# Kernel optimization log

Hardware: AMD Instinct MI355X
Metric: run time of the kernel (lower is better)

Reference implementation:

```python
import jax, jax.numpy as jnp
import numpy as np

N, F_NODE, DIM, H, K, OUT, L = 200000, 16, 3, 128, 20, 4, 4


def setup_inputs() -> dict:
    key = jax.random.key(0)
    ks = jax.random.split(key, 10)
    x = jax.random.normal(ks[0], (N, F_NODE), jnp.float32)
    pos = jax.random.normal(ks[1], (N, DIM), jnp.float32)
    y = jax.random.normal(ks[2], (DIM,), jnp.float32)
    # eigenvector-like basis, roughly orthonormal columns scale
    phi = jax.random.normal(ks[3], (N, K), jnp.float32) / np.sqrt(N).astype(np.float32)
    # torch Linear convention: W is [out, in], y = x @ W.T + b
    lift_w = jax.random.normal(ks[4], (H, F_NODE + 2 * DIM), jnp.float32) * 0.05
    lift_b = jnp.zeros((H,), jnp.float32)
    lin_w = jax.random.normal(ks[5], (L, H, H), jnp.float32) * 0.05  # per-layer, bias=False
    kernel = jax.random.normal(ks[6], (L, K, H, H), jnp.float32) * 0.05
    lower_w = jax.random.normal(ks[7], (OUT, H), jnp.float32) * 0.05
    lower_b = jnp.zeros((OUT,), jnp.float32)
    return dict(x=x, pos=pos, y=y, phi=phi, lift_w=lift_w, lift_b=lift_b,
                lin_w=lin_w, kernel=kernel, lower_w=lower_w, lower_b=lower_b)


def reference(x, pos, y, phi, lift_w, lift_b, lin_w, kernel, lower_w, lower_b):
    # lift: concat node feats, positions, broadcast global y -> [N, F_NODE+2*DIM]
    h = jnp.concatenate([x, pos, y * jnp.ones_like(pos)], axis=1) @ lift_w.T + lift_b
    # pinv(phi) is identical every layer in the original; compute once. [K, N]
    phi_pinv = jnp.linalg.pinv(phi)
    for l in range(L):
        v = phi_pinv @ h                              # [K, H] spectral coefficients
        rv = jnp.einsum('kij,kj->ki', kernel[l], v)   # batched mode matvec (= nested vmap)
        h = jax.nn.elu(h @ lin_w[l].T + phi @ rv)     # [N, H]
    return h @ lower_w.T + lower_b                    # [N, OUT]
```

## Files before the change

kernel.cpp:

```cpp
#include <hip/hip_runtime.h>
#include <math.h>

#define Nn 200000
#define NT 3125

typedef __attribute__((ext_vector_type(8))) short short8;
typedef __attribute__((ext_vector_type(16))) float floatx16;

#define SWZ4(row, g) (((g) ^ ((row) & 7)) << 2)

__device__ __forceinline__ unsigned rnbf(float x) {
    unsigned u = __builtin_bit_cast(unsigned, x);
    return (u + 0x7fffu + ((u >> 16) & 1u)) >> 16;
}
__device__ __forceinline__ float asf(unsigned u) { return __builtin_bit_cast(float, u); }
__device__ __forceinline__ unsigned packf(float x) {
    unsigned hb = rnbf(x);
    float fh = asf(hb << 16);
    unsigned lb = rnbf(x - fh);
    return hb | (lb << 16);
}
__device__ __forceinline__ float unpackf(unsigned p) {
    return asf(p << 16) + asf(p & 0xffff0000u);
}
__device__ __forceinline__ void permsplit(const unsigned* e, short8& hi, short8& lo) {
    uint4 h, l;
    h.x = __builtin_amdgcn_perm(e[1], e[0], 0x05040100u);
    h.y = __builtin_amdgcn_perm(e[3], e[2], 0x05040100u);
    h.z = __builtin_amdgcn_perm(e[5], e[4], 0x05040100u);
    h.w = __builtin_amdgcn_perm(e[7], e[6], 0x05040100u);
    l.x = __builtin_amdgcn_perm(e[1], e[0], 0x07060302u);
    l.y = __builtin_amdgcn_perm(e[3], e[2], 0x07060302u);
    l.z = __builtin_amdgcn_perm(e[5], e[4], 0x07060302u);
    l.w = __builtin_amdgcn_perm(e[7], e[6], 0x07060302u);
    hi = __builtin_bit_cast(short8, h);
    lo = __builtin_bit_cast(short8, l);
}
__device__ __forceinline__ void permsplit2(uint4 q0, uint4 q1, short8& hi, short8& lo) {
    unsigned e[8] = { q0.x, q0.y, q0.z, q0.w, q1.x, q1.y, q1.z, q1.w };
    permsplit(e, hi, lo);
}

__device__ __forceinline__ void pt_accum(const unsigned* As, const unsigned* Ph,
                                         float* __restrict__ PTc_blk, int t) {
    int lane = t & 63, w = t >> 6;
    int ln = lane & 31, hw = lane >> 5;
    int j0 = w * 32;
    floatx16 ap;
#pragma unroll
    for (int i = 0; i < 16; i++) ap[i] = 0.f;
#pragma unroll
    for (int ks = 0; ks < 4; ks++) {
        unsigned pa[8], e[8];
#pragma unroll
        for (int j = 0; j < 8; j++) {
            int node = ks * 16 + 8 * hw + j;
            pa[j] = Ph[node * 32 + SWZ4(node, ln >> 2) + (ln & 3)];
            int col = j0 + ln;
            e[j] = As[node * 128 + SWZ4(node, col >> 2) + (col & 3)];
        }
        short8 a_hi, a_lo, b_hi, b_lo;
        permsplit(pa, a_hi, a_lo);
        permsplit(e, b_hi, b_lo);
        ap = __builtin_amdgcn_mfma_f32_32x32x16_bf16(a_hi, b_hi, ap, 0, 0, 0);
        ap = __builtin_amdgcn_mfma_f32_32x32x16_bf16(a_lo, b_hi, ap, 0, 0, 0);
        ap = __builtin_amdgcn_mfma_f32_32x32x16_bf16(a_hi, b_lo, ap, 0, 0, 0);
    }
#pragma unroll
    for (int r = 0; r < 16; r++) {
        int mode = (r & 3) + 8 * (r >> 2) + 4 * hw;
        if (mode < 20) unsafeAtomicAdd(&PTc_blk[mode * 128 + j0 + ln], ap[r]);
    }
}

__global__ void ptreduce_k(const float* __restrict__ PTc, float* __restrict__ PT) {
    int j = blockIdx.x * 128 + threadIdx.x;
    float s0 = 0.f, s1 = 0.f, s2 = 0.f, s3 = 0.f;
#pragma unroll
    for (int c = 0; c < 64; c += 4) {
        s0 += PTc[(size_t)c * 2560 + j];
        s1 += PTc[(size_t)(c + 1) * 2560 + j];
        s2 += PTc[(size_t)(c + 2) * 2560 + j];
        s3 += PTc[(size_t)(c + 3) * 2560 + j];
    }
    PT[j] = (s0 + s1) + (s2 + s3);
}

__global__ void bias_fold_k(const float* __restrict__ y, const float* __restrict__ lw,
                            const float* __restrict__ lb, float* __restrict__ b2) {
    int j = threadIdx.x;
    float s = lb[j];
#pragma unroll
    for (int d = 0; d < 3; d++) s += y[d] * lw[j * 22 + 19 + d];
    b2[j] = s;
}

__global__ void wsplit_k(const float* __restrict__ lw, const float* __restrict__ low_w,
                         unsigned short* __restrict__ Wh, unsigned short* __restrict__ Wl,
                         unsigned short* __restrict__ LWh, unsigned short* __restrict__ LWl) {
    int i = blockIdx.x * 256 + threadIdx.x;
    float w;
    unsigned short *ph, *pl;
    int idx;
    if (i < 65536) { w = lw[i]; ph = Wh; pl = Wl; idx = i; }
    else           { w = low_w[i - 65536]; ph = LWh; pl = LWl; idx = i - 65536; }
    unsigned hb = rnbf(w);
    float fh = asf(hb << 16);
    unsigned lb = rnbf(w - fh);
    ph[idx] = (unsigned short)hb;
    pl[idx] = (unsigned short)lb;
}

__global__ __launch_bounds__(256) void lift_k(const float* __restrict__ x,
                                              const float* __restrict__ pos,
                                              const float* __restrict__ phi,
                                              const float* __restrict__ lw,
                                              const float* __restrict__ b2,
                                              unsigned* __restrict__ hpk,
                                              float* __restrict__ PTc) {
    __shared__ union {
        struct { float xs[64][21]; float Wc[20][132]; } a;
        unsigned As[64 * 128];
    } sm;
    __shared__ unsigned Ph[64 * 32];
    int t = threadIdx.x;
    int n0 = blockIdx.x * 64;
    {
        int n = t >> 2, f4 = (t & 3) * 4;
        float4 xv = *(const float4*)(x + (size_t)(n0 + n) * 16 + f4);
        sm.a.xs[n][f4 + 0] = xv.x; sm.a.xs[n][f4 + 1] = xv.y;
        sm.a.xs[n][f4 + 2] = xv.z; sm.a.xs[n][f4 + 3] = xv.w;
    }
    if (t < 192) { int n = t / 3, d = t % 3; sm.a.xs[n][16 + d] = pos[(size_t)(n0 + n) * 3 + d]; }
    if (t < 64) sm.a.xs[t][19] = 1.f;
    for (int idx = t; idx < 2560; idx += 256) {
        int k = idx >> 7, j = idx & 127;
        sm.a.Wc[k][j] = (k < 19) ? lw[j * 22 + k] : b2[j];
    }
    for (int idx = t; idx < 2048; idx += 256) {
        int row = idx >> 5, kk = idx & 31;
        float pv = (kk < 20) ? phi[(size_t)(n0 + row) * 20 + kk] : 0.f;
        Ph[row * 32 + SWZ4(row, kk >> 2) + (kk & 3)] = packf(pv);
    }
    __syncthreads();
    int tx = t & 31, ty = t >> 5, i0 = tx * 4;
    float acc[8][4];
#pragma unroll
    for (int m = 0; m < 8; m++)
#pragma unroll
        for (int c = 0; c < 4; c++) acc[m][c] = 0.f;
#pragma unroll 4
    for (int k = 0; k < 20; k++) {
        float4 w = *(const float4*)&sm.a.Wc[k][i0];
#pragma unroll
        for (int m = 0; m < 8; m++) {
            float a = sm.a.xs[ty + 8 * m][k];
            acc[m][0] += a * w.x; acc[m][1] += a * w.y;
            acc[m][2] += a * w.z; acc[m][3] += a * w.w;
        }
    }
    __syncthreads();
#pragma unroll
    for (int m = 0; m < 8; m++) {
        uint4 o;
        o.x = packf(acc[m][0]); o.y = packf(acc[m][1]);
        o.z = packf(acc[m][2]); o.w = packf(acc[m][3]);
        int row = ty + 8 * m;
        *(uint4*)&hpk[(size_t)(n0 + row) * 128 + i0] = o;
        *(uint4*)&sm.As[row * 128 + SWZ4(row, tx)] = o;
    }
    __syncthreads();
    pt_accum(sm.As, Ph, PTc + (size_t)(blockIdx.x & 63) * 2560, t);
}

__global__ void gram_k(const float* __restrict__ phi, float* __restrict__ G) {
    __shared__ float ph[64 * 20];
    int t = threadIdx.x;
    int i0 = t / 20, j0 = t % 20;
    int p1 = t + 256;
    int i1 = p1 / 20, j1 = p1 % 20;
    float a0 = 0.f, a1 = 0.f;
    for (int tile = blockIdx.x; tile < NT; tile += gridDim.x) {
        const float* src = phi + tile * 1280;
        for (int idx = t; idx < 1280; idx += 256) ph[idx] = src[idx];
        __syncthreads();
        for (int n = 0; n < 64; n++) {
            const float* r = ph + n * 20;
            a0 += r[i0] * r[j0];
            if (p1 < 400) a1 += r[i1] * r[j1];
        }
        __syncthreads();
    }
    unsafeAtomicAdd(&G[t], a0);
    if (p1 < 400) unsafeAtomicAdd(&G[p1], a1);
}

__global__ void ginv_k(const float* __restrict__ G, float* __restrict__ Gi) {
    __shared__ float A[20][40];
    __shared__ float colp[20];
    __shared__ float piv;
    int t = threadIdx.x;
    for (int idx = t; idx < 400; idx += 64) {
        int r = idx / 20, c = idx % 20;
        A[r][c] = G[idx];
        A[r][c + 20] = (r == c) ? 1.f : 0.f;
    }
    __syncthreads();
    for (int p = 0; p < 20; p++) {
        if (t == 0) piv = 1.f / A[p][p];
        __syncthreads();
        for (int c = t; c < 40; c += 64) A[p][c] *= piv;
        __syncthreads();
        if (t < 20) colp[t] = A[t][p];
        __syncthreads();
        for (int e = t; e < 800; e += 64) {
            int r = e / 40, c = e % 40;
            if (r != p) A[r][c] -= colp[r] * A[p][c];
        }
        __syncthreads();
    }
    for (int idx = t; idx < 400; idx += 64) {
        int r = idx / 20, c = idx % 20;
        Gi[idx] = A[r][c + 20];
    }
}

__global__ void rv_k(const float* __restrict__ Gi, const float* __restrict__ PT,
                     const float* __restrict__ kern_l,
                     unsigned short* __restrict__ RVh, unsigned short* __restrict__ RVl) {
    __shared__ __align__(16) float v[128];
    __shared__ float part[128];
    int k = blockIdx.x;
    int t = threadIdx.x;
    if (t < 128) {
        const float* gr = Gi + k * 20;
        float s = 0.f;
#pragma unroll
        for (int m = 0; m < 20; m++) s += gr[m] * PT[m * 128 + t];
        v[t] = s;
    }
    __syncthreads();
    int i = t & 127, half = t >> 7;
    const float* kr = kern_l + (size_t)(k * 128 + i) * 128 + half * 64;
    const float* vk = v + half * 64;
    float acc = 0.f;
#pragma unroll 4
    for (int jj = 0; jj < 64; jj += 4) {
        float4 kv = *(const float4*)(kr + jj);
        float4 vv = *(const float4*)(vk + jj);
        acc += kv.x * vv.x + kv.y * vv.y + kv.z * vv.z + kv.w * vv.w;
    }
    if (half) part[i] = acc;
    __syncthreads();
    if (!half) {
        float rv = acc + part[i];
        unsigned hb = rnbf(rv);
        float fh = asf(hb << 16);
        unsigned lb = rnbf(rv - fh);
        RVh[i * 32 + k] = (unsigned short)hb;
        RVl[i * 32 + k] = (unsigned short)lb;
    }
}

__global__ __launch_bounds__(256, 4) void update_k(unsigned* __restrict__ hpk,
                                                   const float* __restrict__ phi,
                                                   const unsigned short* __restrict__ Wh,
                                                   const unsigned short* __restrict__ Wl,
                                                   const unsigned short* __restrict__ RVh,
                                                   const unsigned short* __restrict__ RVl,
                                                   float* __restrict__ ptn,
                                                   const unsigned short* __restrict__ LWh,
                                                   const unsigned short* __restrict__ LWl,
                                                   const float* __restrict__ low_b,
                                                   float* __restrict__ outp) {
    __shared__ __align__(16) unsigned As[64 * 128];
    __shared__ __align__(16) unsigned Ph[64 * 32];
    int t = threadIdx.x;
    int n0 = blockIdx.x * 64;
    for (int idx = t; idx < 2048; idx += 256) {
        int row = idx >> 5, g = idx & 31;
        uint4 v = *(const uint4*)(hpk + (size_t)(n0 + row) * 128 + g * 4);
        *(uint4*)&As[row * 128 + SWZ4(row, g)] = v;
    }
    for (int idx = t; idx < 2048; idx += 256) {
        int row = idx >> 5, kk = idx & 31;
        float pv = (kk < 20) ? phi[(size_t)(n0 + row) * 20 + kk] : 0.f;
        Ph[row * 32 + SWZ4(row, kk >> 2) + (kk & 3)] = packf(pv);
    }
    __syncthreads();

    int lane = t & 63, w = t >> 6;
    int ln = lane & 31, hw = lane >> 5;
    int r0 = (w >> 1) * 32, ct0 = (w & 1) * 64;
    int arow = r0 + ln;

    floatx16 acc0, acc1;
#pragma unroll
    for (int i = 0; i < 16; i++) { acc0[i] = 0.f; acc1[i] = 0.f; }

    const unsigned short* whp0 = Wh + (size_t)(ct0 + ln) * 128 + 8 * hw;
    const unsigned short* wlp0 = Wl + (size_t)(ct0 + ln) * 128 + 8 * hw;
    const unsigned short* whp1 = whp0 + 32 * 128;
    const unsigned short* wlp1 = wlp0 + 32 * 128;
    const unsigned* abase = As + arow * 128;

    uint4 wh0c = *(const uint4*)(whp0), wl0c = *(const uint4*)(wlp0);
    uint4 wh1c = *(const uint4*)(whp1), wl1c = *(const uint4*)(wlp1);
    uint4 aq0c = *(const uint4*)(abase + SWZ4(arow, 2 * hw));
    uint4 aq1c = *(const uint4*)(abase + SWZ4(arow, 2 * hw + 1));
#pragma unroll
    for (int ks = 0; ks < 8; ks++) {
        uint4 wh0n, wl0n, wh1n, wl1n, aq0n, aq1n;
        if (ks < 7) {
            int k1 = (ks + 1) * 16;
            int ga = 4 * (ks + 1) + 2 * hw;
            wh0n = *(const uint4*)(whp0 + k1); wl0n = *(const uint4*)(wlp0 + k1);
            wh1n = *(const uint4*)(whp1 + k1); wl1n = *(const uint4*)(wlp1 + k1);
            aq0n = *(const uint4*)(abase + SWZ4(arow, ga));
            aq1n = *(const uint4*)(abase + SWZ4(arow, ga + 1));
        }
        short8 a_hi, a_lo;
        permsplit2(aq0c, aq1c, a_hi, a_lo);
        short8 b0h = __builtin_bit_cast(short8, wh0c);
        short8 b0l = __builtin_bit_cast(short8, wl0c);
        short8 b1h = __builtin_bit_cast(short8, wh1c);
        short8 b1l = __builtin_bit_cast(short8, wl1c);
        acc0 = __builtin_amdgcn_mfma_f32_32x32x16_bf16(a_hi, b0h, acc0, 0, 0, 0);
        acc0 = __builtin_amdgcn_mfma_f32_32x32x16_bf16(a_lo, b0h, acc0, 0, 0, 0);
        acc0 = __builtin_amdgcn_mfma_f32_32x32x16_bf16(a_hi, b0l, acc0, 0, 0, 0);
        acc1 = __builtin_amdgcn_mfma_f32_32x32x16_bf16(a_hi, b1h, acc1, 0, 0, 0);
        acc1 = __builtin_amdgcn_mfma_f32_32x32x16_bf16(a_lo, b1h, acc1, 0, 0, 0);
        acc1 = __builtin_amdgcn_mfma_f32_32x32x16_bf16(a_hi, b1l, acc1, 0, 0, 0);
        if (ks < 7) {
            wh0c = wh0n; wl0c = wl0n; wh1c = wh1n; wl1c = wl1n;
            aq0c = aq0n; aq1c = aq1n;
        }
    }

    const unsigned* pbase = Ph + arow * 32;
#pragma unroll
    for (int ks = 0; ks < 2; ks++) {
        int k0 = ks * 16;
        int gr = 4 * ks + 2 * hw;
        uint4 q0 = *(const uint4*)(pbase + SWZ4(arow, gr));
        uint4 q1 = *(const uint4*)(pbase + SWZ4(arow, gr + 1));
        short8 a_hi, a_lo;
        permsplit2(q0, q1, a_hi, a_lo);
        short8 b0h = __builtin_bit_cast(short8, *(const uint4*)(RVh + (size_t)(ct0 + ln) * 32 + k0 + 8 * hw));
        short8 b0l = __builtin_bit_cast(short8, *(const uint4*)(RVl + (size_t)(ct0 + ln) * 32 + k0 + 8 * hw));
        short8 b1h = __builtin_bit_cast(short8, *(const uint4*)(RVh + (size_t)(ct0 + 32 + ln) * 32 + k0 + 8 * hw));
        short8 b1l = __builtin_bit_cast(short8, *(const uint4*)(RVl + (size_t)(ct0 + 32 + ln) * 32 + k0 + 8 * hw));
        acc0 = __builtin_amdgcn_mfma_f32_32x32x16_bf16(a_hi, b0h, acc0, 0, 0, 0);
        acc0 = __builtin_amdgcn_mfma_f32_32x32x16_bf16(a_lo, b0h, acc0, 0, 0, 0);
        acc0 = __builtin_amdgcn_mfma_f32_32x32x16_bf16(a_hi, b0l, acc0, 0, 0, 0);
        acc1 = __builtin_amdgcn_mfma_f32_32x32x16_bf16(a_hi, b1h, acc1, 0, 0, 0);
        acc1 = __builtin_amdgcn_mfma_f32_32x32x16_bf16(a_lo, b1h, acc1, 0, 0, 0);
        acc1 = __builtin_amdgcn_mfma_f32_32x32x16_bf16(a_hi, b1l, acc1, 0, 0, 0);
    }

    unsigned p0[16], p1[16];
#pragma unroll
    for (int r = 0; r < 16; r++) {
        float v0 = acc0[r];
        v0 = v0 > 0.f ? v0 : __expf(v0) - 1.f;
        p0[r] = packf(v0);
        float v1 = acc1[r];
        v1 = v1 > 0.f ? v1 : __expf(v1) - 1.f;
        p1[r] = packf(v1);
    }
    if (!outp) {
#pragma unroll
        for (int r = 0; r < 16; r++) {
            int row = (r & 3) + 8 * (r >> 2) + 4 * hw;
            size_t base = (size_t)(n0 + r0 + row) * 128;
            hpk[base + ct0 + ln] = p0[r];
            hpk[base + ct0 + 32 + ln] = p1[r];
        }
    }
    if (ptn || outp) {
        __syncthreads();
#pragma unroll
        for (int r = 0; r < 16; r++) {
            int row = r0 + (r & 3) + 8 * (r >> 2) + 4 * hw;
            int c0 = ct0 + ln, c1 = ct0 + 32 + ln;
            As[row * 128 + SWZ4(row, c0 >> 2) + (c0 & 3)] = p0[r];
            As[row * 128 + SWZ4(row, c1 >> 2) + (c1 & 3)] = p1[r];
        }
        __syncthreads();
        if (outp) {
            float* scr = (float*)Ph;
            int kh = w & 1;
            floatx16 ap;
#pragma unroll
            for (int i = 0; i < 16; i++) ap[i] = 0.f;
#pragma unroll
            for (int kk = 0; kk < 4; kk++) {
                int ks = kh * 4 + kk;
                int ga = 4 * ks + 2 * hw;
                uint4 q0 = *(const uint4*)(abase + SWZ4(arow, ga));
                uint4 q1 = *(const uint4*)(abase + SWZ4(arow, ga + 1));
                short8 a_hi, a_lo;
                permsplit2(q0, q1, a_hi, a_lo);
                short8 bh = { 0, 0, 0, 0, 0, 0, 0, 0 };
                short8 bl = { 0, 0, 0, 0, 0, 0, 0, 0 };
                if (ln < 4) {
                    bh = __builtin_bit_cast(short8, *(const uint4*)(LWh + ln * 128 + ks * 16 + 8 * hw));
                    bl = __builtin_bit_cast(short8, *(const uint4*)(LWl + ln * 128 + ks * 16 + 8 * hw));
                }
                ap = __builtin_amdgcn_mfma_f32_32x32x16_bf16(a_hi, bh, ap, 0, 0, 0);
                ap = __builtin_amdgcn_mfma_f32_32x32x16_bf16(a_lo, bh, ap, 0, 0, 0);
                ap = __builtin_amdgcn_mfma_f32_32x32x16_bf16(a_hi, bl, ap, 0, 0, 0);
            }
            if (kh == 1 && ln < 4) {
#pragma unroll
                for (int r = 0; r < 16; r++) {
                    int row = (r & 3) + 8 * (r >> 2) + 4 * hw;
                    scr[(w >> 1) * 128 + row * 4 + ln] = ap[r];
                }
            }
            __syncthreads();
            if (kh == 0 && ln < 4) {
                float b = low_b[ln];
#pragma unroll
                for (int r = 0; r < 16; r++) {
                    int row = (r & 3) + 8 * (r >> 2) + 4 * hw;
                    float s = ap[r] + scr[(w >> 1) * 128 + row * 4 + ln] + b;
                    outp[(size_t)(n0 + r0 + row) * 4 + ln] = s;
                }
            }
        } else {
            pt_accum(As, Ph, ptn + (size_t)(blockIdx.x & 63) * 2560, t);
        }
    }
}

extern "C" void kernel_launch(void* const* d_in, const int* in_sizes, int n_in,
                              void* d_out, int out_size, void* d_ws, size_t ws_size,
                              hipStream_t stream) {
    (void)in_sizes; (void)n_in; (void)out_size; (void)ws_size;
    const float* x       = (const float*)d_in[0];
    const float* pos     = (const float*)d_in[1];
    const float* y       = (const float*)d_in[2];
    const float* phi     = (const float*)d_in[3];
    const float* lift_w  = (const float*)d_in[4];
    const float* lift_b  = (const float*)d_in[5];
    const float* lin_w   = (const float*)d_in[6];
    const float* kern    = (const float*)d_in[7];
    const float* lower_w = (const float*)d_in[8];
    const float* lower_b = (const float*)d_in[9];
    float* out = (float*)d_out;

    char* ws = (char*)d_ws;
    unsigned* hpk = (unsigned*)ws;
    size_t off = (size_t)Nn * 128 * 4;
    float* b2  = (float*)(ws + off);       off += 512;
    float* G   = (float*)(ws + off);       off += 1600;
    float* Gi  = (float*)(ws + off);       off += 1600;
    off = (off + 15) & ~(size_t)15;
    float* PT  = (float*)(ws + off);       off += 10240;
    float* PTc = (float*)(ws + off);       off += 64 * 2560 * 4;
    unsigned short* W_hi = (unsigned short*)(ws + off);  off += 131072;
    unsigned short* W_lo = (unsigned short*)(ws + off);  off += 131072;
    unsigned short* RVh  = (unsigned short*)(ws + off);  off += 8192;
    unsigned short* RVl  = (unsigned short*)(ws + off);  off += 8192;
    unsigned short* LWh  = (unsigned short*)(ws + off);  off += 1024;
    unsigned short* LWl  = (unsigned short*)(ws + off);  off += 1024;

    hipMemsetAsync(G, 0, 1600, stream);
    hipMemsetAsync(PTc, 0, 64 * 2560 * 4, stream);
    hipMemsetAsync(RVh, 0, 8192, stream);
    hipMemsetAsync(RVl, 0, 8192, stream);
    bias_fold_k<<<1, 128, 0, stream>>>(y, lift_w, lift_b, b2);
    wsplit_k<<<258, 256, 0, stream>>>(lin_w, lower_w, W_hi, W_lo, LWh, LWl);
    lift_k<<<NT, 256, 0, stream>>>(x, pos, phi, lift_w, b2, hpk, PTc);
    gram_k<<<256, 256, 0, stream>>>(phi, G);
    ginv_k<<<1, 64, 0, stream>>>(G, Gi);
    ptreduce_k<<<20, 128, 0, stream>>>(PTc, PT);

    for (int l = 0; l < 4; l++) {
        rv_k<<<20, 256, 0, stream>>>(Gi, PT, kern + (size_t)l * 20 * 128 * 128, RVh, RVl);
        float* ptc = (l < 3) ? PTc : (float*)nullptr;
        if (ptc) hipMemsetAsync(ptc, 0, 64 * 2560 * 4, stream);
        update_k<<<NT, 256, 0, stream>>>(hpk, phi, W_hi + (size_t)l * 16384,
                                         W_lo + (size_t)l * 16384, RVh, RVl, ptc,
                                         LWh, LWl, lower_b,
                                         (l == 3) ? out : (float*)nullptr);
        if (ptc) ptreduce_k<<<20, 128, 0, stream>>>(PTc, PT);
    }
}
```

Before: 619.7 us.

## Use 512-thread blocks in update kernel with one 32x32 tile per wave

The update kernel now runs 8 waves per 64-node block instead of 4. Each wave computes a single 32x32 output tile, so it needs one accumulator instead of two and drops the explicit register double-buffering of the weight and activation loads. The spectral projection accumulation is split across all 8 waves by node halves, and the final lowering step is restricted to the first 4 waves. This aims to raise parallelism and lower register pressure per wave, at the cost of more atomics in the projection and losing software prefetch of the operand loads.

```diff
diff --git a/kernel.cpp b/kernel.cpp
--- a/kernel.cpp
+++ b/kernel.cpp
@@ -51,6 +51,40 @@
     for (int i = 0; i < 16; i++) ap[i] = 0.f;
 #pragma unroll
     for (int ks = 0; ks < 4; ks++) {
+        unsigned pa[8], e[8];
+#pragma unroll
+        for (int j = 0; j < 8; j++) {
+            int node = ks * 16 + 8 * hw + j;
+            pa[j] = Ph[node * 32 + SWZ4(node, ln >> 2) + (ln & 3)];
+            int col = j0 + ln;
+            e[j] = As[node * 128 + SWZ4(node, col >> 2) + (col & 3)];
+        }
+        short8 a_hi, a_lo, b_hi, b_lo;
+        permsplit(pa, a_hi, a_lo);
+        permsplit(e, b_hi, b_lo);
+        ap = __builtin_amdgcn_mfma_f32_32x32x16_bf16(a_hi, b_hi, ap, 0, 0, 0);
+        ap = __builtin_amdgcn_mfma_f32_32x32x16_bf16(a_lo, b_hi, ap, 0, 0, 0);
+        ap = __builtin_amdgcn_mfma_f32_32x32x16_bf16(a_hi, b_lo, ap, 0, 0, 0);
+    }
+#pragma unroll
+    for (int r = 0; r < 16; r++) {
+        int mode = (r & 3) + 8 * (r >> 2) + 4 * hw;
+        if (mode < 20) unsafeAtomicAdd(&PTc_blk[mode * 128 + j0 + ln], ap[r]);
+    }
+}
+
+__device__ __forceinline__ void pt_accum8(const unsigned* As, const unsigned* Ph,
+                                          float* __restrict__ PTc_blk, int t) {
+    int lane = t & 63, w = t >> 6;
+    int ln = lane & 31, hw = lane >> 5;
+    int j0 = (w & 3) * 32;
+    int nh = w >> 2;
+    floatx16 ap;
+#pragma unroll
+    for (int i = 0; i < 16; i++) ap[i] = 0.f;
+#pragma unroll
+    for (int ks2 = 0; ks2 < 2; ks2++) {
+        int ks = nh * 2 + ks2;
         unsigned pa[8], e[8];
 #pragma unroll
         for (int j = 0; j < 8; j++) {
@@ -262,7 +296,7 @@
     }
 }
 
-__global__ __launch_bounds__(256, 4) void update_k(unsigned* __restrict__ hpk,
+__global__ __launch_bounds__(512, 8) void update_k(unsigned* __restrict__ hpk,
                                                    const float* __restrict__ phi,
                                                    const unsigned short* __restrict__ Wh,
                                                    const unsigned short* __restrict__ Wl,
@@ -277,12 +311,12 @@
     __shared__ __align__(16) unsigned Ph[64 * 32];
     int t = threadIdx.x;
     int n0 = blockIdx.x * 64;
-    for (int idx = t; idx < 2048; idx += 256) {
+    for (int idx = t; idx < 2048; idx += 512) {
         int row = idx >> 5, g = idx & 31;
         uint4 v = *(const uint4*)(hpk + (size_t)(n0 + row) * 128 + g * 4);
         *(uint4*)&As[row * 128 + SWZ4(row, g)] = v;
     }
-    for (int idx = t; idx < 2048; idx += 256) {
+    for (int idx = t; idx < 2048; idx += 512) {
         int row = idx >> 5, kk = idx & 31;
         float pv = (kk < 20) ? phi[(size_t)(n0 + row) * 20 + kk] : 0.f;
         Ph[row * 32 + SWZ4(row, kk >> 2) + (kk & 3)] = packf(pv);
@@ -291,50 +325,32 @@
 
     int lane = t & 63, w = t >> 6;
     int ln = lane & 31, hw = lane >> 5;
-    int r0 = (w >> 1) * 32, ct0 = (w & 1) * 64;
+    int r0 = (w >> 2) * 32, ct0 = (w & 3) * 32;
     int arow = r0 + ln;
 
-    floatx16 acc0, acc1;
-#pragma unroll
-    for (int i = 0; i < 16; i++) { acc0[i] = 0.f; acc1[i] = 0.f; }
-
-    const unsigned short* whp0 = Wh + (size_t)(ct0 + ln) * 128 + 8 * hw;
-    const unsigned short* wlp0 = Wl + (size_t)(ct0 + ln) * 128 + 8 * hw;
-    const unsigned short* whp1 = whp0 + 32 * 128;
-    const unsigned short* wlp1 = wlp0 + 32 * 128;
+    floatx16 acc;
+#pragma unroll
+    for (int i = 0; i < 16; i++) acc[i] = 0.f;
+
+    const unsigned short* whp = Wh + (size_t)(ct0 + ln) * 128 + 8 * hw;
+    const unsigned short* wlp = Wl + (size_t)(ct0 + ln) * 128 + 8 * hw;
     const unsigned* abase = As + arow * 128;
 
-    uint4 wh0c = *(const uint4*)(whp0), wl0c = *(const uint4*)(wlp0);
-    uint4 wh1c = *(const uint4*)(whp1), wl1c = *(const uint4*)(wlp1);
-    uint4 aq0c = *(const uint4*)(abase + SWZ4(arow, 2 * hw));
-    uint4 aq1c = *(const uint4*)(abase + SWZ4(arow, 2 * hw + 1));
 #pragma unroll
     for (int ks = 0; ks < 8; ks++) {
-        uint4 wh0n, wl0n, wh1n, wl1n, aq0n, aq1n;
-        if (ks < 7) {
-            int k1 = (ks + 1) * 16;
-            int ga = 4 * (ks + 1) + 2 * hw;
-            wh0n = *(const uint4*)(whp0 + k1); wl0n = *(const uint4*)(wlp0 + k1);
-            wh1n = *(const uint4*)(whp1 + k1); wl1n = *(const uint4*)(wlp1 + k1);
-            aq0n = *(const uint4*)(abase + SWZ4(arow, ga));
-            aq1n = *(const uint4*)(abase + SWZ4(arow, ga + 1));
-        }
+        int k0 = ks * 16;
+        int ga = 4 * ks + 2 * hw;
+        uint4 aq0 = *(const uint4*)(abase + SWZ4(arow, ga));
+        uint4 aq1 = *(const uint4*)(abase + SWZ4(arow, ga + 1));
+        uint4 wh = *(const uint4*)(whp + k0);
+        uint4 wl = *(const uint4*)(wlp + k0);
         short8 a_hi, a_lo;
-        permsplit2(aq0c, aq1c, a_hi, a_lo);
-        short8 b0h = __builtin_bit_cast(short8, wh0c);
-        short8 b0l = __builtin_bit_cast(short8, wl0c);
-        short8 b1h = __builtin_bit_cast(short8, wh1c);
-        short8 b1l = __builtin_bit_cast(short8, wl1c);
-        acc0 = __builtin_amdgcn_mfma_f32_32x32x16_bf16(a_hi, b0h, acc0, 0, 0, 0);
-        acc0 = __builtin_amdgcn_mfma_f32_32x32x16_bf16(a_lo, b0h, acc0, 0, 0, 0);
-        acc0 = __builtin_amdgcn_mfma_f32_32x32x16_bf16(a_hi, b0l, acc0, 0, 0, 0);
-        acc1 = __builtin_amdgcn_mfma_f32_32x32x16_bf16(a_hi, b1h, acc1, 0, 0, 0);
-        acc1 = __builtin_amdgcn_mfma_f32_32x32x16_bf16(a_lo, b1h, acc1, 0, 0, 0);
-        acc1 = __builtin_amdgcn_mfma_f32_32x32x16_bf16(a_hi, b1l, acc1, 0, 0, 0);
-        if (ks < 7) {
-            wh0c = wh0n; wl0c = wl0n; wh1c = wh1n; wl1c = wl1n;
-            aq0c = aq0n; aq1c = aq1n;
-        }
+        permsplit2(aq0, aq1, a_hi, a_lo);
+        short8 bh = __builtin_bit_cast(short8, wh);
+        short8 bl = __builtin_bit_cast(short8, wl);
+        acc = __builtin_amdgcn_mfma_f32_32x32x16_bf16(a_hi, bh, acc, 0, 0, 0);
+        acc = __builtin_amdgcn_mfma_f32_32x32x16_bf16(a_lo, bh, acc, 0, 0, 0);
+        acc = __builtin_amdgcn_mfma_f32_32x32x16_bf16(a_hi, bl, acc, 0, 0, 0);
     }
 
     const unsigned* pbase = Ph + arow * 32;
@@ -346,35 +362,25 @@
         uint4 q1 = *(const uint4*)(pbase + SWZ4(arow, gr + 1));
         short8 a_hi, a_lo;
         permsplit2(q0, q1, a_hi, a_lo);
-        short8 b0h = __builtin_bit_cast(short8, *(const uint4*)(RVh + (size_t)(ct0 + ln) * 32 + k0 + 8 * hw));
-        short8 b0l = __builtin_bit_cast(short8, *(const uint4*)(RVl + (size_t)(ct0 + ln) * 32 + k0 + 8 * hw));
-        short8 b1h = __builtin_bit_cast(short8, *(const uint4*)(RVh + (size_t)(ct0 + 32 + ln) * 32 + k0 + 8 * hw));
-        short8 b1l = __builtin_bit_cast(short8, *(const uint4*)(RVl + (size_t)(ct0 + 32 + ln) * 32 + k0 + 8 * hw));
-        acc0 = __builtin_amdgcn_mfma_f32_32x32x16_bf16(a_hi, b0h, acc0, 0, 0, 0);
-        acc0 = __builtin_amdgcn_mfma_f32_32x32x16_bf16(a_lo, b0h, acc0, 0, 0, 0);
-        acc0 = __builtin_amdgcn_mfma_f32_32x32x16_bf16(a_hi, b0l, acc0, 0, 0, 0);
-        acc1 = __builtin_amdgcn_mfma_f32_32x32x16_bf16(a_hi, b1h, acc1, 0, 0, 0);
-        acc1 = __builtin_amdgcn_mfma_f32_32x32x16_bf16(a_lo, b1h, acc1, 0, 0, 0);
-        acc1 = __builtin_amdgcn_mfma_f32_32x32x16_bf16(a_hi, b1l, acc1, 0, 0, 0);
-    }
-
-    unsigned p0[16], p1[16];
+        short8 bh = __builtin_bit_cast(short8, *(const uint4*)(RVh + (size_t)(ct0 + ln) * 32 + k0 + 8 * hw));
+        short8 bl = __builtin_bit_cast(short8, *(const uint4*)(RVl + (size_t)(ct0 + ln) * 32 + k0 + 8 * hw));
+        acc = __builtin_amdgcn_mfma_f32_32x32x16_bf16(a_hi, bh, acc, 0, 0, 0);
+        acc = __builtin_amdgcn_mfma_f32_32x32x16_bf16(a_lo, bh, acc, 0, 0, 0);
+        acc = __builtin_amdgcn_mfma_f32_32x32x16_bf16(a_hi, bl, acc, 0, 0, 0);
+    }
+
+    unsigned p0[16];
 #pragma unroll
     for (int r = 0; r < 16; r++) {
-        float v0 = acc0[r];
+        float v0 = acc[r];
         v0 = v0 > 0.f ? v0 : __expf(v0) - 1.f;
         p0[r] = packf(v0);
-        float v1 = acc1[r];
-        v1 = v1 > 0.f ? v1 : __expf(v1) - 1.f;
-        p1[r] = packf(v1);
     }
     if (!outp) {
 #pragma unroll
         for (int r = 0; r < 16; r++) {
             int row = (r & 3) + 8 * (r >> 2) + 4 * hw;
-            size_t base = (size_t)(n0 + r0 + row) * 128;
-            hpk[base + ct0 + ln] = p0[r];
-            hpk[base + ct0 + 32 + ln] = p1[r];
+            hpk[(size_t)(n0 + r0 + row) * 128 + ct0 + ln] = p0[r];
         }
     }
     if (ptn || outp) {
@@ -382,36 +388,39 @@
 #pragma unroll
         for (int r = 0; r < 16; r++) {
             int row = r0 + (r & 3) + 8 * (r >> 2) + 4 * hw;
-            int c0 = ct0 + ln, c1 = ct0 + 32 + ln;
+            int c0 = ct0 + ln;
             As[row * 128 + SWZ4(row, c0 >> 2) + (c0 & 3)] = p0[r];
-            As[row * 128 + SWZ4(row, c1 >> 2) + (c1 & 3)] = p1[r];
         }
         __syncthreads();
         if (outp) {
             float* scr = (float*)Ph;
-            int kh = w & 1;
+            int r0o = (w >> 1) * 32, kh = w & 1;
+            int arow2 = r0o + ln;
+            const unsigned* ab2 = As + arow2 * 128;
             floatx16 ap;
 #pragma unroll
             for (int i = 0; i < 16; i++) ap[i] = 0.f;
-#pragma unroll
-            for (int kk = 0; kk < 4; kk++) {
-                int ks = kh * 4 + kk;
-                int ga = 4 * ks + 2 * hw;
-                uint4 q0 = *(const uint4*)(abase + SWZ4(arow, ga));
-                uint4 q1 = *(const uint4*)(abase + SWZ4(arow, ga + 1));
-                short8 a_hi, a_lo;
-                permsplit2(q0, q1, a_hi, a_lo);
-                short8 bh = { 0, 0, 0, 0, 0, 0, 0, 0 };
-                short8 bl = { 0, 0, 0, 0, 0, 0, 0, 0 };
-                if (ln < 4) {
-                    bh = __builtin_bit_cast(short8, *(const uint4*)(LWh + ln * 128 + ks * 16 + 8 * hw));
-                    bl = __builtin_bit_cast(short8, *(const uint4*)(LWl + ln * 128 + ks * 16 + 8 * hw));
+            if (w < 4) {
+#pragma unroll
+                for (int kk = 0; kk < 4; kk++) {
+                    int ks = kh * 4 + kk;
+                    int ga = 4 * ks + 2 * hw;
+                    uint4 q0 = *(const uint4*)(ab2 + SWZ4(arow2, ga));
+                    uint4 q1 = *(const uint4*)(ab2 + SWZ4(arow2, ga + 1));
+                    short8 a_hi, a_lo;
+                    permsplit2(q0, q1, a_hi, a_lo);
+                    short8 bh = { 0, 0, 0, 0, 0, 0, 0, 0 };
+                    short8 bl = { 0, 0, 0, 0, 0, 0, 0, 0 };
+                    if (ln < 4) {
+                        bh = __builtin_bit_cast(short8, *(const uint4*)(LWh + ln * 128 + ks * 16 + 8 * hw));
+                        bl = __builtin_bit_cast(short8, *(const uint4*)(LWl + ln * 128 + ks * 16 + 8 * hw));
+                    }
+                    ap = __builtin_amdgcn_mfma_f32_32x32x16_bf16(a_hi, bh, ap, 0, 0, 0);
+                    ap = __builtin_amdgcn_mfma_f32_32x32x16_bf16(a_lo, bh, ap, 0, 0, 0);
+                    ap = __builtin_amdgcn_mfma_f32_32x32x16_bf16(a_hi, bl, ap, 0, 0, 0);
                 }
-                ap = __builtin_amdgcn_mfma_f32_32x32x16_bf16(a_hi, bh, ap, 0, 0, 0);
-                ap = __builtin_amdgcn_mfma_f32_32x32x16_bf16(a_lo, bh, ap, 0, 0, 0);
-                ap = __builtin_amdgcn_mfma_f32_32x32x16_bf16(a_hi, bl, ap, 0, 0, 0);
             }
-            if (kh == 1 && ln < 4) {
+            if (w < 4 && kh == 1 && ln < 4) {
 #pragma unroll
                 for (int r = 0; r < 16; r++) {
                     int row = (r & 3) + 8 * (r >> 2) + 4 * hw;
@@ -419,17 +428,17 @@
                 }
             }
             __syncthreads();
-            if (kh == 0 && ln < 4) {
+            if (w < 4 && kh == 0 && ln < 4) {
                 float b = low_b[ln];
 #pragma unroll
                 for (int r = 0; r < 16; r++) {
                     int row = (r & 3) + 8 * (r >> 2) + 4 * hw;
                     float s = ap[r] + scr[(w >> 1) * 128 + row * 4 + ln] + b;
-                    outp[(size_t)(n0 + r0 + row) * 4 + ln] = s;
+                    outp[(size_t)(n0 + r0o + row) * 4 + ln] = s;
                 }
             }
         } else {
-            pt_accum(As, Ph, ptn + (size_t)(blockIdx.x & 63) * 2560, t);
+            pt_accum8(As, Ph, ptn + (size_t)(blockIdx.x & 63) * 2560, t);
         }
     }
 }
@@ -481,7 +490,7 @@
         rv_k<<<20, 256, 0, stream>>>(Gi, PT, kern + (size_t)l * 20 * 128 * 128, RVh, RVl);
         float* ptc = (l < 3) ? PTc : (float*)nullptr;
         if (ptc) hipMemsetAsync(ptc, 0, 64 * 2560 * 4, stream);
-        update_k<<<NT, 256, 0, stream>>>(hpk, phi, W_hi + (size_t)l * 16384,
+        update_k<<<NT, 512, 0, stream>>>(hpk, phi, W_hi + (size_t)l * 16384,
                                          W_lo + (size_t)l * 16384, RVh, RVl, ptc,
                                          LWh, LWl, lower_b,
                                          (l == 3) ? out : (float*)nullptr);
```

Measured after the change: 642.5 us. +3.7%, slower.
